# Performance work log

Hardware: AMD Instinct MI355X
Metric: run time of the kernel (lower is better)

Reference implementation:

```python
import jax, jax.numpy as jnp
import numpy as np

SR = 16000
N_TAPS = 10
MIN_F = 50.0
MAX_F = 2000.0


def setup_inputs() -> dict:
    key = jax.random.key(0)
    k1, k2 = jax.random.split(key)
    x = jax.random.normal(k1, (8, 1, 32000), dtype=jnp.float32)
    # raw f params as in the module: 3*(rand*2-1) in [-3, 3]
    f = 3.0 * (jax.random.uniform(k2, (128, 1), dtype=jnp.float32) * 2.0 - 1.0)
    a = jnp.full((128, 1), 0.9, dtype=jnp.float32)
    return {"x": x, "f": f, "a": a}


def _comb(x, f_raw, a):
    # scaling_function (min_freq/max_freq branch, no bins):
    # f = min_freq * (max_freq/min_freq) ** sigmoid(f_raw)
    fratio = MAX_F / MIN_F
    f = MIN_F * fratio ** jax.nn.sigmoid(f_raw)  # [O, I] fundamental freq in Hz

    B, I, T = x.shape
    O = f.shape[0]
    D = SR / f  # [O, I] fractional delay in samples (one period)
    n = jnp.arange(T, dtype=x.dtype)
    ci = jnp.arange(I)[None, :, None]  # channel index for gather, [1, I, 1]

    acc = jnp.zeros((B, O, T), dtype=x.dtype)
    # y[b,o,t] = sum_i sum_{k=0}^{n_taps-1} a[o,i]^k * lerp(x[b,i, t - k*D[o,i]])
    for k in range(N_TAPS):
        pos = n[None, None, :] - k * D[:, :, None]  # [O, I, T] fractional read positions
        i0 = jnp.floor(pos)
        frac = (pos - i0).astype(x.dtype)
        valid = (i0 >= 0).astype(x.dtype)  # causal: zero before signal start
        i0i = jnp.clip(i0.astype(jnp.int32), 0, T - 1)
        i1i = jnp.clip(i0i + 1, 0, T - 1)
        x0 = x[:, ci, i0i]  # [B, O, I, T]
        x1 = x[:, ci, i1i]  # [B, O, I, T]
        tap = (x0 * (1.0 - frac) + x1 * frac) * valid
        acc = acc + jnp.sum((a ** k)[None, :, :, None] * tap, axis=2)
    return acc


def reference(x, f, a):
    # use_bias=False -> b = 0, gain g unused in forward
    return _comb(x, f, a)
```

## Files before the change

### kernel.cpp

```cpp
#include <hip/hip_runtime.h>
#include <math.h>

#define T_LEN 32000
#define B_N 8
#define O_N 128
#define NTAPS 10
#define TILE_T 256
#define PAD 2944
#define NSTAGE (TILE_T + PAD + 1)
#define OCHUNK 16

__global__ __launch_bounds__(128) void comb_params_kernel(
    const float* __restrict__ f, const float* __restrict__ a,
    float* __restrict__ tp) {
  int o = threadIdx.x;
  double fr = (double)f[o];
  double sig = 1.0 / (1.0 + exp(-fr));
  float ff = (float)(50.0 * pow(40.0, sig));
  float D = 16000.0f / ff;
  float av = a[o];
  for (int k = 0; k < NTAPS; ++k) {
    tp[o * 20 + k] = (float)k * D;
    tp[o * 20 + 10 + k] = (float)pow((double)av, (double)k);
  }
}

template <bool SAFE>
__device__ __forceinline__ void comb_body(const float* __restrict__ tp,
                                          float* __restrict__ outp,
                                          const float* sx, int oc,
                                          float t_f, int base_g) {
#pragma unroll 1
  for (int oi = 0; oi < OCHUNK; ++oi) {
    const float* __restrict__ p = tp + (oc + oi) * 20;
    float acc = 0.0f;
#pragma unroll
    for (int k = 0; k < NTAPS; ++k) {
      float kD = p[k];
      float ak = p[10 + k];
      float pos = t_f - kD;
      float frac = __builtin_amdgcn_fractf(pos);
      int idx = (int)pos - base_g;
      float x0 = sx[idx];
      float x1 = sx[idx + 1];
      float tap = fmaf(frac, x1 - x0, x0);
      if (!SAFE) tap = (pos >= 0.0f) ? tap : 0.0f;
      acc = fmaf(ak, tap, acc);
    }
    outp[(size_t)oi * T_LEN] = acc;
  }
}

__global__ __launch_bounds__(256) void comb_main_kernel(
    const float* __restrict__ x, const float* __restrict__ tp,
    float* __restrict__ out) {
  __shared__ float sx[NSTAGE];
  int t0 = blockIdx.x * TILE_T;
  int b = blockIdx.y;
  int oc = blockIdx.z * OCHUNK;
  const float* __restrict__ xrow = x + b * T_LEN;
  int base_g = t0 - PAD;

  for (int j = threadIdx.x; j < NSTAGE; j += 256) {
    int g = base_g + j;
    float v = 0.0f;
    if (g >= 0) v = xrow[g < T_LEN - 1 ? g : T_LEN - 1];
    sx[j] = v;
  }
  __syncthreads();

  int t = t0 + threadIdx.x;
  float* outp = out + ((size_t)b * O_N + oc) * T_LEN + t;
  float t_f = (float)t;
  if (t0 >= PAD)
    comb_body<true>(tp, outp, sx, oc, t_f, base_g);
  else
    comb_body<false>(tp, outp, sx, oc, t_f, base_g);
}

extern "C" void kernel_launch(void* const* d_in, const int* in_sizes, int n_in,
                              void* d_out, int out_size, void* d_ws,
                              size_t ws_size, hipStream_t stream) {
  const float* x = (const float*)d_in[0];
  const float* f = (const float*)d_in[1];
  const float* a = (const float*)d_in[2];
  float* out = (float*)d_out;
  float* tp = (float*)d_ws;

  comb_params_kernel<<<1, 128, 0, stream>>>(f, a, tp);

  dim3 grid(T_LEN / TILE_T, B_N, O_N / OCHUNK);
  comb_main_kernel<<<grid, 256, 0, stream>>>(x, tp, out);
}
```

Measured before the change: 177.0 us.

## Process five time samples per thread and vectorize interior shared staging

Each block now covers 1280 time samples instead of 256, and every thread computes 5 outputs per channel. The large 2944-sample history halo is therefore staged once per 1280 outputs rather than once per 256, and the per-channel tap parameters are reused across five outputs. Interior blocks load the shared tile with float4 copies without bounds checks. The cost is more registers per thread and a grid five times smaller in the time dimension (25x8x8 blocks), which may reduce occupancy and load balance.

```diff
diff --git a/kernel.cpp b/kernel.cpp
--- a/kernel.cpp
+++ b/kernel.cpp
@@ -5,9 +5,11 @@
 #define B_N 8
 #define O_N 128
 #define NTAPS 10
-#define TILE_T 256
+#define TILE_T 1280
+#define NT 5
 #define PAD 2944
 #define NSTAGE (TILE_T + PAD + 1)
+#define NSTAGE_AL ((NSTAGE + 3) & ~3)
 #define OCHUNK 16
 
 __global__ __launch_bounds__(128) void comb_params_kernel(
@@ -29,53 +31,71 @@
 __device__ __forceinline__ void comb_body(const float* __restrict__ tp,
                                           float* __restrict__ outp,
                                           const float* sx, int oc,
-                                          float t_f, int base_g) {
+                                          const float* tf, int base_g) {
 #pragma unroll 1
   for (int oi = 0; oi < OCHUNK; ++oi) {
     const float* __restrict__ p = tp + (oc + oi) * 20;
-    float acc = 0.0f;
+    float acc[NT];
 #pragma unroll
+    for (int j = 0; j < NT; ++j) acc[j] = 0.0f;
     for (int k = 0; k < NTAPS; ++k) {
       float kD = p[k];
       float ak = p[10 + k];
-      float pos = t_f - kD;
-      float frac = __builtin_amdgcn_fractf(pos);
-      int idx = (int)pos - base_g;
-      float x0 = sx[idx];
-      float x1 = sx[idx + 1];
-      float tap = fmaf(frac, x1 - x0, x0);
-      if (!SAFE) tap = (pos >= 0.0f) ? tap : 0.0f;
-      acc = fmaf(ak, tap, acc);
+#pragma unroll
+      for (int j = 0; j < NT; ++j) {
+        float pos = tf[j] - kD;
+        float frac = __builtin_amdgcn_fractf(pos);
+        int idx = (int)pos - base_g;
+        float x0 = sx[idx];
+        float x1 = sx[idx + 1];
+        float tap = fmaf(frac, x1 - x0, x0);
+        if (!SAFE) tap = (pos >= 0.0f) ? tap : 0.0f;
+        acc[j] = fmaf(ak, tap, acc[j]);
+      }
     }
-    outp[(size_t)oi * T_LEN] = acc;
+#pragma unroll
+    for (int j = 0; j < NT; ++j)
+      outp[(size_t)oi * T_LEN + 256 * j] = acc[j];
   }
 }
 
 __global__ __launch_bounds__(256) void comb_main_kernel(
     const float* __restrict__ x, const float* __restrict__ tp,
     float* __restrict__ out) {
-  __shared__ float sx[NSTAGE];
-  int t0 = blockIdx.x * TILE_T;
+  __shared__ float sx[NSTAGE_AL];
+  int bx = blockIdx.x;
+  int t0 = bx * TILE_T;
   int b = blockIdx.y;
   int oc = blockIdx.z * OCHUNK;
   const float* __restrict__ xrow = x + b * T_LEN;
   int base_g = t0 - PAD;
+  int tid = threadIdx.x;
 
-  for (int j = threadIdx.x; j < NSTAGE; j += 256) {
-    int g = base_g + j;
-    float v = 0.0f;
-    if (g >= 0) v = xrow[g < T_LEN - 1 ? g : T_LEN - 1];
-    sx[j] = v;
+  if (bx >= 3 && bx <= 23) {
+    float4* s4 = (float4*)sx;
+    const float4* g4 = (const float4*)(xrow + base_g);
+#pragma unroll 1
+    for (int j = tid; j < NSTAGE_AL / 4; j += 256) s4[j] = g4[j];
+  } else {
+#pragma unroll 1
+    for (int j = tid; j < NSTAGE_AL; j += 256) {
+      int g = base_g + j;
+      float v = 0.0f;
+      if (g >= 0) v = xrow[g < T_LEN - 1 ? g : T_LEN - 1];
+      sx[j] = v;
+    }
   }
   __syncthreads();
 
-  int t = t0 + threadIdx.x;
-  float* outp = out + ((size_t)b * O_N + oc) * T_LEN + t;
-  float t_f = (float)t;
+  float tf[NT];
+#pragma unroll
+  for (int j = 0; j < NT; ++j) tf[j] = (float)(t0 + tid + 256 * j);
+  float* outp = out + ((size_t)b * O_N + oc) * T_LEN + t0 + tid;
+
   if (t0 >= PAD)
-    comb_body<true>(tp, outp, sx, oc, t_f, base_g);
+    comb_body<true>(tp, outp, sx, oc, tf, base_g);
   else
-    comb_body<false>(tp, outp, sx, oc, t_f, base_g);
+    comb_body<false>(tp, outp, sx, oc, tf, base_g);
 }
 
 extern "C" void kernel_launch(void* const* d_in, const int* in_sizes, int n_in,
```

Result: slower. 197.1 us (+11.4%).
